# Kernel tuning notes

Measured on AMD Instinct MI355X. Metric: run time of the kernel, lower is better.

Reference implementation:

```python
import jax, jax.numpy as jnp
import numpy as np

DIM = 512
HEADS = 8
DIM_HEAD = 64
INNER = HEADS * DIM_HEAD  # 512
B, N = 32, 512
LN_EPS = 1e-5


def setup_inputs() -> dict:
    key = jax.random.key(0)
    ks = jax.random.split(key, 8)
    inp = {
        "q": jax.random.normal(ks[0], (B, N, DIM), jnp.float32),
        "k": jax.random.normal(ks[1], (B, N, DIM), jnp.float32),
        "v": jax.random.normal(ks[2], (B, N, DIM), jnp.float32),
        "ln_w": jnp.ones((DIM,), jnp.float32),
        "ln_b": jnp.zeros((DIM,), jnp.float32),
        "W_in": jax.random.normal(ks[3], (DIM, INNER), jnp.float32) / np.sqrt(DIM),
        "W_out": jax.random.normal(ks[4], (INNER, DIM), jnp.float32) / np.sqrt(INNER),
        "b_out": jnp.zeros((DIM,), jnp.float32),
        "cov_w_raw": jnp.float32(0.6),
        "var_w_raw": jnp.float32(0.2),
    }
    return inp


def _project(x, ln_w, ln_b, W_in):
    # LayerNorm(dim) -> Linear(dim, inner, bias=False) -> 'b n (h d) -> h b n d'
    mu = jnp.mean(x, axis=-1, keepdims=True)
    var = jnp.var(x, axis=-1, keepdims=True)  # biased, as in nn.LayerNorm
    xn = (x - mu) / jnp.sqrt(var + LN_EPS) * ln_w + ln_b
    f = xn @ W_in  # [B, N, inner]
    Bq, Nq, _ = f.shape
    f = f.reshape(Bq, Nq, HEADS, DIM_HEAD)
    return jnp.transpose(f, (2, 0, 1, 3))  # [h, B, N, d]


def reference(q, k, v, ln_w, ln_b, W_in, W_out, b_out, cov_w_raw, var_w_raw):
    f_q = _project(q, ln_w, ln_b, W_in)  # [h, B, N, d]
    f_k = _project(k, ln_w, ln_b, W_in)
    f_v = _project(v, ln_w, ln_b, W_in)

    d = f_q.shape[-1]

    # cosine similarity: (q . k) / (||q|| ||k||)
    dots = jnp.einsum('hbnd,hbmd->hbnm', f_q, f_k)
    qn = jnp.linalg.norm(f_q, axis=-1)  # [h, B, N]
    kn = jnp.linalg.norm(f_k, axis=-1)  # [h, B, M]
    cosine_sim = dots / (qn[..., :, None] * kn[..., None, :])

    # basic covariance component: centered dot / d
    qc = f_q - jnp.mean(f_q, axis=-1, keepdims=True)
    kc = f_k - jnp.mean(f_k, axis=-1, keepdims=True)
    cov_component = jnp.einsum('hbnd,hbmd->hbnm', qc, kc) / d

    # variance component: outer product of per-token variances (unbiased) / d
    q_var = jnp.var(f_q, axis=-1, ddof=1)  # [h, B, N]
    k_var = jnp.var(f_k, axis=-1, ddof=1)  # [h, B, M]
    var_component = (q_var[..., :, None] * k_var[..., None, :]) / d

    cov_w = jax.nn.sigmoid(cov_w_raw)
    var_w = jax.nn.sigmoid(var_w_raw)
    cos_w = 1.0 - cov_w - var_w

    scores = cos_w * cosine_sim + cov_w * cov_component + var_w * var_component
    out = jnp.einsum('hbnm,hbmd->hbnd', scores, f_v)  # no softmax in cosine variant

    # 'h b n d -> b n (h d)'
    out = jnp.transpose(out, (1, 2, 0, 3)).reshape(out.shape[1], out.shape[2], INNER)
    return out @ W_out + b_out
```

## Files before the change

### kernel.cpp

```cpp
#include <hip/hip_runtime.h>
#include <stdint.h>

using u16 = unsigned short;
using u32 = unsigned int;
using bf16x8 = __bf16 __attribute__((ext_vector_type(8)));
using f32x4  = float __attribute__((ext_vector_type(4)));

__device__ __forceinline__ float bflo(u32 u){ return __uint_as_float(u << 16); }
__device__ __forceinline__ float bfhi(u32 u){ return __uint_as_float(u & 0xffff0000u); }
__device__ __forceinline__ u16 f2bf(float f){
  u32 u = __float_as_uint(f);
  u += 0x7fffu + ((u >> 16) & 1u);
  return (u16)(u >> 16);
}
__device__ __forceinline__ u32 pk2(float a, float b){
  return (u32)f2bf(a) | ((u32)f2bf(b) << 16);
}
__device__ __forceinline__ void gload16(const void* g, void* l){
  __builtin_amdgcn_global_load_lds(
      (const __attribute__((address_space(1))) void*)(uintptr_t)(g),
      (__attribute__((address_space(3))) void*)(uintptr_t)(l), 16, 0, 0);
}

__global__ __launch_bounds__(256) void prepcast_k(
    const float* __restrict__ q, const float* __restrict__ k, const float* __restrict__ v,
    const float* __restrict__ lnw, const float* __restrict__ lnb,
    u16* __restrict__ xnq, u16* __restrict__ xnk, u16* __restrict__ xnv,
    const float* __restrict__ Win, const float* __restrict__ Wout,
    u16* __restrict__ WinT, u16* __restrict__ WoutT){
  __shared__ float tile[32][33];
  if (blockIdx.x >= 12288){
    int bi = blockIdx.x - 12288;
    int bz = bi >> 8; bi &= 255;
    int bx = bi & 15, by = bi >> 4;
    const float* src = bz ? Wout : Win;
    u16* dst = bz ? WoutT : WinT;
    int tx = threadIdx.x & 31, ty = threadIdx.x >> 5;
    int c0 = bx * 32, r0 = by * 32;
#pragma unroll
    for (int i = 0; i < 4; ++i)
      tile[ty + i*8][tx] = src[(size_t)(r0 + ty + i*8)*512 + c0 + tx];
    __syncthreads();
#pragma unroll
    for (int i = 0; i < 4; ++i)
      dst[(size_t)(c0 + ty + i*8)*512 + r0 + tx] = f2bf(tile[tx][ty + i*8]);
    return;
  }
  int row = blockIdx.x * 4 + (threadIdx.x >> 6);
  int l = threadIdx.x & 63;
  const float* x = (row < 16384) ? q : (row < 32768) ? k : v;
  u16* xo = (row < 16384) ? xnq : (row < 32768) ? xnk : xnv;
  int r = row & 16383;
  const float* rp = x + (size_t)r * 512 + l*8;
  float4 a = *(const float4*)rp, c = *(const float4*)(rp + 4);
  float sum = ((a.x+a.y)+(a.z+a.w)) + ((c.x+c.y)+(c.z+c.w));
  float ss  = ((a.x*a.x+a.y*a.y)+(a.z*a.z+a.w*a.w)) + ((c.x*c.x+c.y*c.y)+(c.z*c.z+c.w*c.w));
#pragma unroll
  for (int off = 32; off; off >>= 1){
    sum += __shfl_xor(sum, off);
    ss  += __shfl_xor(ss,  off);
  }
  float mu = sum * (1.f/512.f);
  float rs = rsqrtf(ss * (1.f/512.f) - mu*mu + 1e-5f);
  float4 w0 = *(const float4*)(lnw + l*8), w1 = *(const float4*)(lnw + l*8 + 4);
  float4 b0 = *(const float4*)(lnb + l*8), b1 = *(const float4*)(lnb + l*8 + 4);
  uint4 pk;
  pk.x = pk2((a.x-mu)*rs*w0.x + b0.x, (a.y-mu)*rs*w0.y + b0.y);
  pk.y = pk2((a.z-mu)*rs*w0.z + b0.z, (a.w-mu)*rs*w0.w + b0.w);
  pk.z = pk2((c.x-mu)*rs*w1.x + b1.x, (c.y-mu)*rs*w1.y + b1.y);
  pk.w = pk2((c.z-mu)*rs*w1.z + b1.z, (c.w-mu)*rs*w1.w + b1.w);
  *(uint4*)((char*)xo + (size_t)r*1024 + l*16) = pk;
}

template<int MAP, int FSTAT>
__device__ __forceinline__ void gemm_body(
    const u16* __restrict__ A, const u16* __restrict__ B,
    u16* __restrict__ C, float* __restrict__ stat, int ldC, int bid,
    char* sA, char* sB){
  const int t = threadIdx.x, w = t >> 6, l = t & 63;
  const int wr = w >> 1, wc = w & 1;
  const int lr = l & 15, lg = l >> 4;
  int bx, by;
  if (MAP == 0){ bx = bid & 127; by = bid >> 7; }
  else { int j = bid >> 3; bx = j & 3; by = (bid & 7) + 8*(j >> 2); }
  const int row0 = bx * 128, col0 = by * 128;
  f32x4 acc[4][4] = {};

  const int sc = t >> 3, k8 = t & 7;
  const int sso = (k8*16) ^ ((sc & 7) << 4);
  const char* Ap = (const char*)A + ((size_t)(row0 + sc) << 10) + sso;
  const char* Bp = (const char*)B + ((size_t)(col0 + sc) << 10) + sso;

  for (int kt = 0; kt < 8; ++kt){
    __syncthreads();
#pragma unroll
    for (int ii = 0; ii < 4; ++ii){
      gload16(Ap + (size_t)ii*32768 + kt*128, sA + ii*4096 + w*1024);
      gload16(Bp + (size_t)ii*32768 + kt*128, sB + ii*4096 + w*1024);
    }
    __syncthreads();
#pragma unroll
    for (int kk = 0; kk < 2; ++kk){
      bf16x8 af[4], bfg[4];
#pragma unroll
      for (int m = 0; m < 4; ++m){
        int r = wr*64 + m*16 + lr;
        af[m] = *(const bf16x8*)(sA + r*128 + ((kk*64 + lg*16) ^ ((r & 7) << 4)));
      }
#pragma unroll
      for (int n = 0; n < 4; ++n){
        int r = wc*64 + n*16 + lr;
        bfg[n] = *(const bf16x8*)(sB + r*128 + ((kk*64 + lg*16) ^ ((r & 7) << 4)));
      }
#pragma unroll
      for (int m = 0; m < 4; ++m)
#pragma unroll
        for (int n = 0; n < 4; ++n)
          acc[m][n] = __builtin_amdgcn_mfma_f32_16x16x32_bf16(af[m], bfg[n], acc[m][n], 0, 0, 0);
    }
  }
  float cs[4] = {}, cs2[4] = {};
#pragma unroll
  for (int m = 0; m < 4; ++m){
#pragma unroll
    for (int q = 0; q < 4; ++q){
      int ri = wr*64 + m*16 + lg*4 + q;
      float fv[4];
#pragma unroll
      for (int n = 0; n < 4; ++n){
        int ci = wc*64 + n*16 + lr;
        fv[n] = acc[m][n][q];
        C[(size_t)(row0 + ri)*ldC + (col0 + ci)] = f2bf(fv[n]);
        if (FSTAT == 2){ cs[n] += fv[n]; cs2[n] += fv[n]*fv[n]; }
      }
      if (FSTAT == 1){
        float s  = (fv[0]+fv[1]) + (fv[2]+fv[3]);
        float s2 = (fv[0]*fv[0]+fv[1]*fv[1]) + (fv[2]*fv[2]+fv[3]*fv[3]);
#pragma unroll
        for (int off = 1; off < 16; off <<= 1){ s += __shfl_xor(s, off); s2 += __shfl_xor(s2, off); }
        if (lr == 0){
          int head = (col0 >> 6) + wc;
          *(float2*)(stat + ((size_t)(row0 + ri)*8 + head)*2) = make_float2(s, s2);
        }
      }
    }
  }
  if (FSTAT == 2){
    int head = (row0 >> 6) + wr;
#pragma unroll
    for (int n = 0; n < 4; ++n){
      float s = cs[n], s2 = cs2[n];
      s += __shfl_xor(s, 16); s2 += __shfl_xor(s2, 16);
      s += __shfl_xor(s, 32); s2 += __shfl_xor(s2, 32);
      if (lg == 0){
        int tok = col0 + wc*64 + n*16 + lr;
        *(float2*)(stat + ((size_t)tok*8 + head)*2) = make_float2(s, s2);
      }
    }
  }
}

__global__ __launch_bounds__(256) void proj_k(
    const u16* __restrict__ xnq, const u16* __restrict__ xnk, const u16* __restrict__ xnv,
    const u16* __restrict__ Wt,
    u16* __restrict__ fq, u16* __restrict__ kT, u16* __restrict__ vT,
    float* __restrict__ qstat, float* __restrict__ kstat){
  __shared__ __align__(16) char sA[16384];
  __shared__ __align__(16) char sB[16384];
  int bid = blockIdx.x;
  if (bid < 512)
    gemm_body<0,1>(xnq, Wt, fq, qstat, 512, bid, sA, sB);
  else if (bid < 1024)
    gemm_body<1,2>(Wt, xnk, kT, kstat, 16384, bid - 512, sA, sB);
  else
    gemm_body<1,0>(Wt, xnv, vT, nullptr, 16384, bid - 1024, sA, sB);
}

__global__ __launch_bounds__(256) void outgemm_k(
    const u16* __restrict__ A, const u16* __restrict__ B,
    float* __restrict__ Cf, const float* __restrict__ bias){
  __shared__ __align__(16) char sA[16384];
  __shared__ __align__(16) char sB[16384];
  const int t = threadIdx.x, w = t >> 6, l = t & 63;
  const int wr = w >> 1, wc = w & 1;
  const int lr = l & 15, lg = l >> 4;
  const int row0 = blockIdx.x * 128, col0 = blockIdx.y * 128;
  f32x4 acc[4][4] = {};

  const int sc = t >> 3, k8 = t & 7;
  const int sso = (k8*16) ^ ((sc & 7) << 4);
  const char* Ap = (const char*)A + ((size_t)(row0 + sc) << 10) + sso;
  const char* Bp = (const char*)B + ((size_t)(col0 + sc) << 10) + sso;

  for (int kt = 0; kt < 8; ++kt){
    __syncthreads();
#pragma unroll
    for (int ii = 0; ii < 4; ++ii){
      gload16(Ap + (size_t)ii*32768 + kt*128, sA + ii*4096 + w*1024);
      gload16(Bp + (size_t)ii*32768 + kt*128, sB + ii*4096 + w*1024);
    }
    __syncthreads();
#pragma unroll
    for (int kk = 0; kk < 2; ++kk){
      bf16x8 af[4], bfg[4];
#pragma unroll
      for (int m = 0; m < 4; ++m){
        int r = wr*64 + m*16 + lr;
        af[m] = *(const bf16x8*)(sA + r*128 + ((kk*64 + lg*16) ^ ((r & 7) << 4)));
      }
#pragma unroll
      for (int n = 0; n < 4; ++n){
        int r = wc*64 + n*16 + lr;
        bfg[n] = *(const bf16x8*)(sB + r*128 + ((kk*64 + lg*16) ^ ((r & 7) << 4)));
      }
#pragma unroll
      for (int m = 0; m < 4; ++m)
#pragma unroll
        for (int n = 0; n < 4; ++n)
          acc[m][n] = __builtin_amdgcn_mfma_f32_16x16x32_bf16(af[m], bfg[n], acc[m][n], 0, 0, 0);
    }
  }
#pragma unroll
  for (int m = 0; m < 4; ++m){
#pragma unroll
    for (int q = 0; q < 4; ++q){
      int r = row0 + wr*64 + m*16 + lg*4 + q;
#pragma unroll
      for (int n = 0; n < 4; ++n){
        int cc = col0 + wc*64 + n*16 + lr;
        Cf[(size_t)r*512 + cc] = acc[m][n][q] + bias[cc];
      }
    }
  }
}

__global__ __launch_bounds__(512) void attn_k(
    const u16* __restrict__ fq, const u16* __restrict__ kT, const u16* __restrict__ vT,
    const float* __restrict__ qstat, const float* __restrict__ kstat,
    u16* __restrict__ ao,
    const float* __restrict__ cwr, const float* __restrict__ vwr){
  __shared__ __align__(16) char smem[131072 + 1664*4];
  float* sStat = (float*)(smem + 131072);
  float* sS1 = sStat + 1536;
  float* sS2 = sStat + 1600;

  const int t = threadIdx.x, w = t >> 6, l = t & 63;
  const int lr = l & 15, lg = l >> 4;
  const int h = blockIdx.x & 7, b = blockIdx.x >> 3;

  float cwv = 1.f/(1.f + __expf(-*cwr));
  float vwv = 1.f/(1.f + __expf(-*vwr));
  float cosw = 1.f - cwv - vwv;

  const char* kTb = (const char*)kT + (size_t)h*64*32768 + (size_t)b*1024;
  const char* vTb = (const char*)vT + (size_t)h*64*32768 + (size_t)b*1024;
#pragma unroll
  for (int ii = 0; ii < 8; ++ii){
    int c = ii*512 + t, d = c >> 6, u = c & 63;
    int so = d*32768 + ((u ^ (d & 7)) << 4);
    gload16(kTb + so, smem + ii*8192 + w*1024);
    gload16(vTb + so, smem + 65536 + ii*8192 + w*1024);
  }
  {
    float2 ksr = *(const float2*)(kstat + ((size_t)(b*512 + t)*8 + h)*2);
    float mk = ksr.x * (1.f/64.f);
    sStat[t]        = rsqrtf(ksr.y);
    sStat[512 + t]  = mk;
    sStat[1024 + t] = (ksr.y - 64.f*mk*mk) * (1.f/63.f);
  }
  __syncthreads();

  const int jt = (w >> 1), itp = (w & 1);
  f32x4 m2acc[2] = {}, m1acc[2] = {};
  {
    const int j = jt*16 + lr;
#pragma unroll
    for (int ks = 0; ks < 16; ++ks){
      int u = ks*4 + lg;
      bf16x8 af = *(const bf16x8*)(smem + 65536 + j*1024 + ((u ^ (j & 7)) << 4));
#pragma unroll
      for (int tt = 0; tt < 2; ++tt){
        int i = (itp*2 + tt)*16 + lr;
        bf16x8 bf = *(const bf16x8*)(smem + i*1024 + ((u ^ (i & 7)) << 4));
        m2acc[tt] = __builtin_amdgcn_mfma_f32_16x16x32_bf16(af, bf, m2acc[tt], 0, 0, 0);
      }
    }
  }
  {
    int j = t >> 3, g = t & 7;
    float p1 = 0.f, p2 = 0.f;
#pragma unroll
    for (int uu = 0; uu < 8; ++uu){
      int ut = g*8 + uu;
      uint4 uv = *(const uint4*)(smem + 65536 + j*1024 + ((ut ^ (j & 7)) << 4));
      int m0 = ut*8;
      float4 mk0 = *(const float4*)(sStat + 512 + m0);
      float4 mk1 = *(const float4*)(sStat + 512 + m0 + 4);
      float4 kv0 = *(const float4*)(sStat + 1024 + m0);
      float4 kv1 = *(const float4*)(sStat + 1024 + m0 + 4);
      float v0=bflo(uv.x),v1=bfhi(uv.x),v2=bflo(uv.y),v3=bfhi(uv.y);
      float v4=bflo(uv.z),v5=bfhi(uv.z),v6=bflo(uv.w),v7=bfhi(uv.w);
      p1 += v0*mk0.x + v1*mk0.y + v2*mk0.z + v3*mk0.w
          + v4*mk1.x + v5*mk1.y + v6*mk1.z + v7*mk1.w;
      p2 += v0*kv0.x + v1*kv0.y + v2*kv0.z + v3*kv0.w
          + v4*kv1.x + v5*kv1.y + v6*kv1.z + v7*kv1.w;
    }
#pragma unroll
    for (int off = 1; off < 8; off <<= 1){ p1 += __shfl_xor(p1, off); p2 += __shfl_xor(p2, off); }
    if (g == 0){ sS1[j] = p1; sS2[j] = p2; }
  }
  __syncthreads();

#pragma unroll
  for (int ii = 0; ii < 32; ++ii){
    int wd = ii*512 + t;
    int d = wd >> 8, o = wd & 255, ud = o >> 2, p = o & 3;
    int m0 = ((ud ^ (d & 7)) << 3) + p*2;
    u32 uv = *(u32*)(smem + wd*4);
    *(u32*)(smem + wd*4) = pk2(bflo(uv)*sStat[m0], bfhi(uv)*sStat[m0+1]);
  }
  __syncthreads();

  {
    const int j = jt*16 + lr;
#pragma unroll
    for (int ks = 0; ks < 16; ++ks){
      int u = ks*4 + lg;
      bf16x8 af = *(const bf16x8*)(smem + 65536 + j*1024 + ((u ^ (j & 7)) << 4));
#pragma unroll
      for (int tt = 0; tt < 2; ++tt){
        int i = (itp*2 + tt)*16 + lr;
        bf16x8 bf = *(const bf16x8*)(smem + i*1024 + ((u ^ (i & 7)) << 4));
        m1acc[tt] = __builtin_amdgcn_mfma_f32_16x16x32_bf16(af, bf, m1acc[tt], 0, 0, 0);
      }
    }
  }
  __syncthreads();

#pragma unroll
  for (int tt = 0; tt < 2; ++tt){
#pragma unroll
    for (int q = 0; q < 4; ++q){
      int j = jt*16 + lg*4 + q;
      int i = (itp*2 + tt)*16 + lr;
      int bo = j*128 + (((i >> 3) ^ (j & 7)) << 4) + (i & 7)*2;
      *(u16*)(smem + bo)        = f2bf(m1acc[tt][q]);
      *(u16*)(smem + 8192 + bo) = f2bf(m2acc[tt][q]);
    }
  }
  const char* fqb = (const char*)fq + (size_t)b*524288 + h*128;
#pragma unroll
  for (int ii = 0; ii < 8; ++ii){
    int c = ii*512 + t, n = c >> 3, u = c & 7;
    gload16(fqb + n*1024 + ((u ^ (n & 7)) << 4), smem + 65536 + ii*8192 + w*1024);
  }
  __syncthreads();

  float s1v[4], s2v[4];
#pragma unroll
  for (int nt = 0; nt < 4; ++nt){ s1v[nt] = sS1[nt*16 + lr]; s2v[nt] = sS2[nt*16 + lr]; }
  const float Bc = cwv * (1.f/64.f);

#pragma unroll
  for (int mt = 0; mt < 4; ++mt){
    f32x4 a1[4] = {}, a2[4] = {};
    const int n = w*64 + mt*16 + lr;
#pragma unroll
    for (int kk = 0; kk < 2; ++kk){
      int u = kk*4 + lg;
      bf16x8 af = *(const bf16x8*)(smem + 65536 + n*128 + ((u ^ (n & 7)) << 4));
#pragma unroll
      for (int nt = 0; nt < 4; ++nt){
        int j = nt*16 + lr;
        bf16x8 b1 = *(const bf16x8*)(smem + j*128 + ((u ^ (j & 7)) << 4));
        bf16x8 b2 = *(const bf16x8*)(smem + 8192 + j*128 + ((u ^ (j & 7)) << 4));
        a1[nt] = __builtin_amdgcn_mfma_f32_16x16x32_bf16(af, b1, a1[nt], 0, 0, 0);
        a2[nt] = __builtin_amdgcn_mfma_f32_16x16x32_bf16(af, b2, a2[nt], 0, 0, 0);
      }
    }
#pragma unroll
    for (int q = 0; q < 4; ++q){
      int nr = w*64 + mt*16 + lg*4 + q;
      float2 qs = *(const float2*)(qstat + ((size_t)(b*512 + nr)*8 + h)*2);
      float mq = qs.x * (1.f/64.f);
      float An = cosw * rsqrtf(qs.y);
      float Cn = -cwv * mq;
      float En = vwv * (1.f/64.f) * ((qs.y - 64.f*mq*mq) * (1.f/63.f));
      char* op = (char*)ao + ((size_t)(b*512 + nr)*512 + h*64)*2;
#pragma unroll
      for (int nt = 0; nt < 4; ++nt){
        float ov = An*a1[nt][q] + Bc*a2[nt][q] + Cn*s1v[nt] + En*s2v[nt];
        *(u16*)(op + (nt*16 + lr)*2) = f2bf(ov);
      }
    }
  }
}

extern "C" void kernel_launch(void* const* d_in, const int* in_sizes, int n_in,
                              void* d_out, int out_size, void* d_ws, size_t ws_size,
                              hipStream_t stream){
  const float* q    = (const float*)d_in[0];
  const float* k    = (const float*)d_in[1];
  const float* v    = (const float*)d_in[2];
  const float* lnw  = (const float*)d_in[3];
  const float* lnb  = (const float*)d_in[4];
  const float* Win  = (const float*)d_in[5];
  const float* Wout = (const float*)d_in[6];
  const float* bout = (const float*)d_in[7];
  const float* cwr  = (const float*)d_in[8];
  const float* vwr  = (const float*)d_in[9];

  char* ws = (char*)d_ws;
  const size_t FB = (size_t)16384 * 512 * 2;
  u16* xnq = (u16*)(ws);
  u16* xnk = (u16*)(ws + FB);
  u16* xnv = (u16*)(ws + 2*FB);
  u16* fq  = (u16*)(ws + 3*FB);
  u16* kT  = (u16*)(ws + 4*FB);
  u16* vT  = (u16*)(ws + 5*FB);
  u16* ao  = (u16*)(ws + 6*FB);
  u16* WinT  = (u16*)(ws + 7*FB);
  u16* WoutT = (u16*)(ws + 7*FB + 524288);
  float* qstat = (float*)d_out;
  float* kstat = qstat + 262144;

  prepcast_k<<<12800, 256, 0, stream>>>(q, k, v, lnw, lnb, xnq, xnk, xnv,
                                        Win, Wout, WinT, WoutT);

  proj_k<<<1536, 256, 0, stream>>>(xnq, xnk, xnv, WinT, fq, kT, vT, qstat, kstat);

  attn_k<<<256, 512, 0, stream>>>(fq, kT, vT, qstat, kstat, ao, cwr, vwr);

  outgemm_k<<<dim3(128,4), 256, 0, stream>>>(ao, WoutT, (float*)d_out, bout);
}
```

Measured before the change: 101.7 us.

## Pipeline output GEMM with 4-stage LDS buffering, split projection launches, recoalesce LayerNorm

The output GEMM now uses a four-buffer LDS ring with 64-byte K slices and explicit vmcnt waits, so global loads for later K steps overlap MFMA work instead of sitting behind two barriers per step. The fused projection kernel is split into three template-specialized launches, one each for q, k and v. The LayerNorm prep now has each lane read two float4s spaced half a row apart and write two 8-byte stores, changing its access pattern. The deeper pipeline raises LDS use to 64KB per block, which can lower occupancy, and the split projections add launch overhead and remove the overlap of q/k/v work within one grid.

```diff
diff --git a/kernel.cpp b/kernel.cpp
--- a/kernel.cpp
+++ b/kernel.cpp
@@ -51,8 +51,9 @@
   const float* x = (row < 16384) ? q : (row < 32768) ? k : v;
   u16* xo = (row < 16384) ? xnq : (row < 32768) ? xnk : xnv;
   int r = row & 16383;
-  const float* rp = x + (size_t)r * 512 + l*8;
-  float4 a = *(const float4*)rp, c = *(const float4*)(rp + 4);
+  const float* rp = x + (size_t)r * 512;
+  float4 a = *(const float4*)(rp + l*4);
+  float4 c = *(const float4*)(rp + 256 + l*4);
   float sum = ((a.x+a.y)+(a.z+a.w)) + ((c.x+c.y)+(c.z+c.w));
   float ss  = ((a.x*a.x+a.y*a.y)+(a.z*a.z+a.w*a.w)) + ((c.x*c.x+c.y*c.y)+(c.z*c.z+c.w*c.w));
 #pragma unroll
@@ -62,18 +63,19 @@
   }
   float mu = sum * (1.f/512.f);
   float rs = rsqrtf(ss * (1.f/512.f) - mu*mu + 1e-5f);
-  float4 w0 = *(const float4*)(lnw + l*8), w1 = *(const float4*)(lnw + l*8 + 4);
-  float4 b0 = *(const float4*)(lnb + l*8), b1 = *(const float4*)(lnb + l*8 + 4);
-  uint4 pk;
-  pk.x = pk2((a.x-mu)*rs*w0.x + b0.x, (a.y-mu)*rs*w0.y + b0.y);
-  pk.y = pk2((a.z-mu)*rs*w0.z + b0.z, (a.w-mu)*rs*w0.w + b0.w);
-  pk.z = pk2((c.x-mu)*rs*w1.x + b1.x, (c.y-mu)*rs*w1.y + b1.y);
-  pk.w = pk2((c.z-mu)*rs*w1.z + b1.z, (c.w-mu)*rs*w1.w + b1.w);
-  *(uint4*)((char*)xo + (size_t)r*1024 + l*16) = pk;
+  float4 w0 = *(const float4*)(lnw + l*4), w1 = *(const float4*)(lnw + 256 + l*4);
+  float4 b0 = *(const float4*)(lnb + l*4), b1 = *(const float4*)(lnb + 256 + l*4);
+  uint2 o1, o2;
+  o1.x = pk2((a.x-mu)*rs*w0.x + b0.x, (a.y-mu)*rs*w0.y + b0.y);
+  o1.y = pk2((a.z-mu)*rs*w0.z + b0.z, (a.w-mu)*rs*w0.w + b0.w);
+  o2.x = pk2((c.x-mu)*rs*w1.x + b1.x, (c.y-mu)*rs*w1.y + b1.y);
+  o2.y = pk2((c.z-mu)*rs*w1.z + b1.z, (c.w-mu)*rs*w1.w + b1.w);
+  *(uint2*)((char*)xo + (size_t)r*1024 + l*8)       = o1;
+  *(uint2*)((char*)xo + (size_t)r*1024 + 512 + l*8) = o2;
 }
 
 template<int MAP, int FSTAT>
-__device__ __forceinline__ void gemm_body(
+__device__ __forceinline__ void gemm_body_s(
     const u16* __restrict__ A, const u16* __restrict__ B,
     u16* __restrict__ C, float* __restrict__ stat, int ldC, int bid,
     char* sA, char* sB){
@@ -160,75 +162,77 @@
   }
 }
 
-__global__ __launch_bounds__(256) void proj_k(
-    const u16* __restrict__ xnq, const u16* __restrict__ xnk, const u16* __restrict__ xnv,
-    const u16* __restrict__ Wt,
-    u16* __restrict__ fq, u16* __restrict__ kT, u16* __restrict__ vT,
-    float* __restrict__ qstat, float* __restrict__ kstat){
+template<int MAP, int FSTAT>
+__global__ __launch_bounds__(256) void projx_k(
+    const u16* __restrict__ A, const u16* __restrict__ B,
+    u16* __restrict__ C, float* __restrict__ stat, int ldC){
   __shared__ __align__(16) char sA[16384];
   __shared__ __align__(16) char sB[16384];
-  int bid = blockIdx.x;
-  if (bid < 512)
-    gemm_body<0,1>(xnq, Wt, fq, qstat, 512, bid, sA, sB);
-  else if (bid < 1024)
-    gemm_body<1,2>(Wt, xnk, kT, kstat, 16384, bid - 512, sA, sB);
-  else
-    gemm_body<1,0>(Wt, xnv, vT, nullptr, 16384, bid - 1024, sA, sB);
+  gemm_body_s<MAP, FSTAT>(A, B, C, stat, ldC, blockIdx.x, sA, sB);
 }
 
 __global__ __launch_bounds__(256) void outgemm_k(
     const u16* __restrict__ A, const u16* __restrict__ B,
     float* __restrict__ Cf, const float* __restrict__ bias){
-  __shared__ __align__(16) char sA[16384];
-  __shared__ __align__(16) char sB[16384];
+  __shared__ __align__(16) char sM[65536];
   const int t = threadIdx.x, w = t >> 6, l = t & 63;
   const int wr = w >> 1, wc = w & 1;
   const int lr = l & 15, lg = l >> 4;
-  const int row0 = blockIdx.x * 128, col0 = blockIdx.y * 128;
+  const int bx = blockIdx.x & 127, by = blockIdx.x >> 7;
+  const int row0 = bx*128, col0 = by*128;
+
+  const int spr = t >> 3, se = (t & 7) ^ (spr & 7);
+  const int srow = spr*2 + (se >> 2), sk16 = se & 3;
+  const char* Ap0 = (const char*)A + ((size_t)(row0 + srow) << 10) + sk16*16;
+  const char* Bp0 = (const char*)B + ((size_t)(col0 + srow) << 10) + sk16*16;
+  const int ldst = w*1024 + l*16;
+
+  const int qf = ((((lr & 1) << 2) | lg) ^ ((lr >> 1) & 7)) * 16;
+  const int afb = wr*4096 + (lr >> 1)*128 + qf;
+  const int bfb = wc*4096 + (lr >> 1)*128 + qf;
+
   f32x4 acc[4][4] = {};
 
-  const int sc = t >> 3, k8 = t & 7;
-  const int sso = (k8*16) ^ ((sc & 7) << 4);
-  const char* Ap = (const char*)A + ((size_t)(row0 + sc) << 10) + sso;
-  const char* Bp = (const char*)B + ((size_t)(col0 + sc) << 10) + sso;
-
-  for (int kt = 0; kt < 8; ++kt){
-    __syncthreads();
-#pragma unroll
-    for (int ii = 0; ii < 4; ++ii){
-      gload16(Ap + (size_t)ii*32768 + kt*128, sA + ii*4096 + w*1024);
-      gload16(Bp + (size_t)ii*32768 + kt*128, sB + ii*4096 + w*1024);
-    }
-    __syncthreads();
-#pragma unroll
-    for (int kk = 0; kk < 2; ++kk){
-      bf16x8 af[4], bfg[4];
-#pragma unroll
-      for (int m = 0; m < 4; ++m){
-        int r = wr*64 + m*16 + lr;
-        af[m] = *(const bf16x8*)(sA + r*128 + ((kk*64 + lg*16) ^ ((r & 7) << 4)));
-      }
-#pragma unroll
-      for (int n = 0; n < 4; ++n){
-        int r = wc*64 + n*16 + lr;
-        bfg[n] = *(const bf16x8*)(sB + r*128 + ((kk*64 + lg*16) ^ ((r & 7) << 4)));
-      }
-#pragma unroll
-      for (int m = 0; m < 4; ++m)
-#pragma unroll
-        for (int n = 0; n < 4; ++n)
-          acc[m][n] = __builtin_amdgcn_mfma_f32_16x16x32_bf16(af[m], bfg[n], acc[m][n], 0, 0, 0);
-    }
-  }
+  auto STAGE = [&](int kt, int buf){
+    char* d = sM + buf*16384;
+    gload16(Ap0 + kt*64,         d + ldst);
+    gload16(Ap0 + 65536 + kt*64, d + 4096 + ldst);
+    gload16(Bp0 + kt*64,         d + 8192 + ldst);
+    gload16(Bp0 + 65536 + kt*64, d + 12288 + ldst);
+  };
+
+  STAGE(0, 0); STAGE(1, 1); STAGE(2, 2);
+#pragma unroll
+  for (int kt = 0; kt < 16; ++kt){
+    if (kt < 14)       asm volatile("s_waitcnt vmcnt(8)" ::: "memory");
+    else if (kt == 14) asm volatile("s_waitcnt vmcnt(4)" ::: "memory");
+    else               asm volatile("s_waitcnt vmcnt(0)" ::: "memory");
+    __builtin_amdgcn_s_barrier();
+    __builtin_amdgcn_sched_barrier(0);
+    if (kt < 13) STAGE(kt + 3, (kt + 3) & 3);
+    const char* aR = sM + (kt & 3)*16384;
+    const char* bR = aR + 8192;
+    bf16x8 af[4], bfg[4];
+#pragma unroll
+    for (int m = 0; m < 4; ++m) af[m]  = *(const bf16x8*)(aR + afb + m*1024);
+#pragma unroll
+    for (int n = 0; n < 4; ++n) bfg[n] = *(const bf16x8*)(bR + bfb + n*1024);
+#pragma unroll
+    for (int m = 0; m < 4; ++m)
+#pragma unroll
+      for (int n = 0; n < 4; ++n)
+        acc[m][n] = __builtin_amdgcn_mfma_f32_16x16x32_bf16(af[m], bfg[n], acc[m][n], 0, 0, 0);
+  }
+
 #pragma unroll
   for (int m = 0; m < 4; ++m){
 #pragma unroll
-    for (int q = 0; q < 4; ++q){
-      int r = row0 + wr*64 + m*16 + lg*4 + q;
+    for (int qq = 0; qq < 4; ++qq){
+      int r = row0 + wr*64 + m*16 + lg*4 + qq;
 #pragma unroll
       for (int n = 0; n < 4; ++n){
         int cc = col0 + wc*64 + n*16 + lr;
-        Cf[(size_t)r*512 + cc] = acc[m][n][q] + bias[cc];
+        Cf[(size_t)r*512 + cc] = acc[m][n][qq] + bias[cc];
       }
     }
   }
@@ -427,9 +431,11 @@
   prepcast_k<<<12800, 256, 0, stream>>>(q, k, v, lnw, lnb, xnq, xnk, xnv,
                                         Win, Wout, WinT, WoutT);
 
-  proj_k<<<1536, 256, 0, stream>>>(xnq, xnk, xnv, WinT, fq, kT, vT, qstat, kstat);
+  projx_k<0,1><<<512, 256, 0, stream>>>(xnq, WinT, fq, qstat, 512);
+  projx_k<1,2><<<512, 256, 0, stream>>>(WinT, xnk, kT, kstat, 16384);
+  projx_k<1,0><<<512, 256, 0, stream>>>(WinT, xnv, vT, nullptr, 16384);
 
   attn_k<<<256, 512, 0, stream>>>(fq, kT, vT, qstat, kstat, ao, cwr, vwr);
 
-  outgemm_k<<<dim3(128,4), 256, 0, stream>>>(ao, WoutT, (float*)d_out, bout);
-}
+  outgemm_k<<<512, 256, 0, stream>>>(ao, WoutT, (float*)d_out, bout);
+}
```

Result: slower. 107.3 us (+5.5%).
